# Performance work log

Measured on AMD Instinct MI355X. Metric: run time of the kernel, lower is better.

## Reference

```python
import jax, jax.numpy as jnp
import numpy as np


def _causal_conv(x, w, b, dilation):
    # x: (B, Cin, N), w: (Cout, Cin, K) -> causal: left-pad (K-1)*dilation
    pad = (w.shape[-1] - 1) * dilation
    y = jax.lax.conv_general_dilated(
        x, w, window_strides=(1,), padding=[(pad, 0)],
        rhs_dilation=(dilation,), dimension_numbers=('NCH', 'OIH', 'NCH'))
    return y + b[None, :, None]


def setup_inputs() -> dict:
    key = jax.random.key(0)
    ks = jax.random.split(key, 8)
    B, N, C, L = 8, 32768, 16, 30
    s = 0.1  # weight scale to avoid gate saturation
    return {
        'x': jax.random.normal(ks[0], (B, N), dtype=jnp.float32) * 1000.0,  # int16-like samples
        'lengths': jax.random.randint(ks[1], (B,), N // 2, N),
        'w0': jax.random.normal(ks[2], (C, 1, 2), dtype=jnp.float32) * s,
        'b0': jnp.zeros((C,), jnp.float32),
        'wf': jax.random.normal(ks[3], (L - 1, C, C, 2), dtype=jnp.float32) * s,
        'bf': jnp.zeros((L - 1, C), jnp.float32),
        'wg': jax.random.normal(ks[4], (L - 1, C, C, 2), dtype=jnp.float32) * s,
        'bg': jnp.zeros((L - 1, C), jnp.float32),
        'wa': jax.random.normal(ks[5], (64, C), dtype=jnp.float32) * s,
        'ba': jnp.zeros((64,), jnp.float32),
        'wo': jax.random.normal(ks[6], (256, 64), dtype=jnp.float32) * s,
        'bo': jnp.zeros((256,), jnp.float32),
    }


def reference(x, lengths, w0, b0, wf, bf, wg, bg, wa, ba, wo, bo):
    L = wf.shape[0] + 1  # total layers (layer 0 is plain causal conv)
    xin = (x / 32768.0)[:, None, :]            # (B,1,N), int16 normalization 65536/2
    out0 = _causal_conv(xin, w0, b0, 1)        # (B,C,N)
    agg = out0                                 # skip aggregate
    h = xin + out0                             # residual input (broadcast 1->C channels)
    for i in range(1, L):                      # fixed small layer count
        d = 2 ** (i % 10)
        f = _causal_conv(h, wf[i - 1], bf[i - 1], d)
        g = _causal_conv(h, wg[i - 1], bg[i - 1], d)
        out = jnp.tanh(f) * jax.nn.sigmoid(g)  # gated activation unit
        agg = agg + out
        h = h + out
    a = jnp.einsum('oc,bcn->bon', wa, jax.nn.relu(agg)) + ba[None, :, None]  # agregate1x1
    o = jnp.einsum('oc,bcn->bon', wo, jax.nn.relu(a)) + bo[None, :, None]    # output1x1
    o = jax.nn.log_softmax(o, axis=1)
    mask = (jnp.arange(o.shape[-1]) < lengths[:, None]).astype(o.dtype)      # (B,N)
    return o * mask[:, None, :]
```

## Files before the change

kernel.cpp:

```cpp
#include <hip/hip_runtime.h>

#define NSEQ 32768
#define NB 8
#define NC 16
#define LBLK 1024
#define LPX (LBLK / 8)
#define QGRD 4096
#define QPX (QGRD / 8)

__device__ __forceinline__ float sigm_f(float x) {
    return __fdividef(1.f, 1.f + __expf(-x));
}
__device__ __forceinline__ float tanh_f(float x) {
    return __fdividef(2.f, 1.f + __expf(-2.f * x)) - 1.f;
}

__global__ __launch_bounds__(256) void k_layer0(
    const float* __restrict__ x, const float* __restrict__ w0,
    const float* __restrict__ b0, float* __restrict__ h)
{
    int bid = blockIdx.x;
    int tid = ((bid & 7) * LPX + (bid >> 3)) * 256 + threadIdx.x;
    int n = tid & (NSEQ - 1);
    const float inv = 1.f / 32768.f;
    float xc = x[tid] * inv;
    float xp = (n >= 1) ? x[tid - 1] * inv : 0.f;
    float v[NC];
#pragma unroll
    for (int c = 0; c < NC; c++) {
        float o = w0[c * 2] * xp + w0[c * 2 + 1] * xc + b0[c];
        v[c] = xc + o;
    }
    float4* ph = (float4*)(h + (size_t)tid * NC);
#pragma unroll
    for (int i = 0; i < 4; i++)
        ph[i] = make_float4(v[i * 4], v[i * 4 + 1], v[i * 4 + 2], v[i * 4 + 3]);
}

__global__ __launch_bounds__(256) void k_layer(
    const float* __restrict__ hin, float* __restrict__ hout,
    const float* __restrict__ wf, const float* __restrict__ bf,
    const float* __restrict__ wg, const float* __restrict__ bg, int d)
{
    int bid = blockIdx.x;
    int lbid = (bid & 7) * QPX + (bid >> 3);
    int t = threadIdx.x;
    int pos = lbid * 64 + (t & 63);
    int q = __builtin_amdgcn_readfirstlane(t >> 6);
    int n = pos & (NSEQ - 1);

    float hc[NC], hp[NC];
    {
        const float4* pc = (const float4*)(hin + (size_t)pos * NC);
#pragma unroll
        for (int i = 0; i < 4; i++) {
            float4 tv = pc[i];
            hc[i * 4] = tv.x; hc[i * 4 + 1] = tv.y; hc[i * 4 + 2] = tv.z; hc[i * 4 + 3] = tv.w;
        }
    }
    if (n >= d) {
        const float4* pp = (const float4*)(hin + (size_t)(pos - d) * NC);
#pragma unroll
        for (int i = 0; i < 4; i++) {
            float4 tv = pp[i];
            hp[i * 4] = tv.x; hp[i * 4 + 1] = tv.y; hp[i * 4 + 2] = tv.z; hp[i * 4 + 3] = tv.w;
        }
    } else {
#pragma unroll
        for (int i = 0; i < NC; i++) hp[i] = 0.f;
    }

    const int c0 = q * 4;
    float f[4], g[4];
#pragma unroll
    for (int j = 0; j < 4; j++) { f[j] = bf[c0 + j]; g[j] = bg[c0 + j]; }

#pragma unroll
    for (int ci = 0; ci < NC; ci++) {
        float xp = hp[ci], xc = hc[ci];
#pragma unroll
        for (int j = 0; j < 4; j++) {
            int co = c0 + j;
            f[j] = fmaf(wf[(co * NC + ci) * 2 + 0], xp, f[j]);
            f[j] = fmaf(wf[(co * NC + ci) * 2 + 1], xc, f[j]);
            g[j] = fmaf(wg[(co * NC + ci) * 2 + 0], xp, g[j]);
            g[j] = fmaf(wg[(co * NC + ci) * 2 + 1], xc, g[j]);
        }
    }

    float v[4];
#pragma unroll
    for (int j = 0; j < 4; j++) {
        float outv = tanh_f(f[j]) * sigm_f(g[j]);
        v[j] = hc[c0 + j] + outv;
    }
    float4* po = (float4*)(hout + (size_t)pos * NC + c0);
    po[0] = make_float4(v[0], v[1], v[2], v[3]);
}

__global__ __launch_bounds__(512, 2) void k_final(
    const float* __restrict__ hfin, const float* __restrict__ x,
    const int* __restrict__ lengths,
    const float* __restrict__ wa, const float* __restrict__ ba,
    const float* __restrict__ wo, const float* __restrict__ bo,
    float* __restrict__ out)
{
    __shared__ float s_r[64][17];
    __shared__ float s_ra[64][65];
    __shared__ float s_red[2][8][64];

    int t = threadIdx.x;
    int p = t & 63;
    int q = __builtin_amdgcn_readfirstlane(t >> 6);
    int blk = blockIdx.x;
    int b = blk >> 9;
    int n0 = (blk & 511) << 6;
    int n = n0 + p;
    size_t pos = (size_t)b * NSEQ + n;
    float xin = x[pos] * (1.f / 32768.f);

    if (q < 4) {
        const float4* ph = (const float4*)(hfin + pos * NC);
        float4 v = ph[q];
        s_r[p][q * 4 + 0] = fmaxf(v.x - xin, 0.f);
        s_r[p][q * 4 + 1] = fmaxf(v.y - xin, 0.f);
        s_r[p][q * 4 + 2] = fmaxf(v.z - xin, 0.f);
        s_r[p][q * 4 + 3] = fmaxf(v.w - xin, 0.f);
    }
    __syncthreads();

    {
        float r[NC];
#pragma unroll
        for (int c = 0; c < NC; c++) r[c] = s_r[p][c];
#pragma unroll
        for (int jj = 0; jj < 8; jj++) {
            int j = q * 8 + jj;
            float acc = ba[j];
#pragma unroll
            for (int c = 0; c < NC; c++) acc = fmaf(wa[j * NC + c], r[c], acc);
            s_ra[p][j] = fmaxf(acc, 0.f);
        }
    }
    __syncthreads();

    float ra[64];
#pragma unroll
    for (int j = 0; j < 64; j++) ra[j] = s_ra[p][j];

    float o[32];
    float m = -1e30f;
#pragma unroll 4
    for (int kk = 0; kk < 32; kk++) {
        int k = q * 32 + kk;
        float acc = bo[k];
#pragma unroll
        for (int j = 0; j < 64; j++) acc = fmaf(wo[k * 64 + j], ra[j], acc);
        o[kk] = acc;
        m = fmaxf(m, acc);
    }
    s_red[0][q][p] = m;
    __syncthreads();
    m = fmaxf(fmaxf(fmaxf(s_red[0][0][p], s_red[0][1][p]),
                    fmaxf(s_red[0][2][p], s_red[0][3][p])),
              fmaxf(fmaxf(s_red[0][4][p], s_red[0][5][p]),
                    fmaxf(s_red[0][6][p], s_red[0][7][p])));
    float s = 0.f;
#pragma unroll
    for (int kk = 0; kk < 32; kk++) s += __expf(o[kk] - m);
    s_red[1][q][p] = s;
    __syncthreads();
    s = ((s_red[1][0][p] + s_red[1][1][p]) + (s_red[1][2][p] + s_red[1][3][p]))
      + ((s_red[1][4][p] + s_red[1][5][p]) + (s_red[1][6][p] + s_red[1][7][p]));
    float lse = m + __logf(s);

    bool valid = n < lengths[b];
    float* po = out + ((size_t)b * 256 + q * 32) * NSEQ + n;
#pragma unroll
    for (int kk = 0; kk < 32; kk++) {
        float v = valid ? (o[kk] - lse) : 0.f;
        __builtin_nontemporal_store(v, &po[(size_t)kk * NSEQ]);
    }
}

extern "C" void kernel_launch(void* const* d_in, const int* in_sizes, int n_in,
                              void* d_out, int out_size, void* d_ws, size_t ws_size,
                              hipStream_t stream) {
    const float* x   = (const float*)d_in[0];
    const int* lens  = (const int*)d_in[1];
    const float* w0  = (const float*)d_in[2];
    const float* b0  = (const float*)d_in[3];
    const float* wf  = (const float*)d_in[4];
    const float* bf  = (const float*)d_in[5];
    const float* wg  = (const float*)d_in[6];
    const float* bg  = (const float*)d_in[7];
    const float* wa  = (const float*)d_in[8];
    const float* ba  = (const float*)d_in[9];
    const float* wo  = (const float*)d_in[10];
    const float* bo  = (const float*)d_in[11];
    float* out = (float*)d_out;

    float* hA = (float*)d_ws;
    float* hB = hA + (size_t)NB * NSEQ * NC;

    k_layer0<<<dim3(LBLK), dim3(256), 0, stream>>>(x, w0, b0, hA);

    float* cur = hA;
    float* nxt = hB;
    for (int i = 1; i <= 29; i++) {
        int d = 1 << (i % 10);
        k_layer<<<dim3(QGRD), dim3(256), 0, stream>>>(cur, nxt,
                                         wf + (size_t)(i - 1) * NC * NC * 2,
                                         bf + (size_t)(i - 1) * NC,
                                         wg + (size_t)(i - 1) * NC * NC * 2,
                                         bg + (size_t)(i - 1) * NC, d);
        float* tmp = cur; cur = nxt; nxt = tmp;
    }

    dim3 fgrd(NB * (NSEQ / 64));
    k_final<<<fgrd, dim3(512), 0, stream>>>(cur, x, lens, wa, ba, wo, bo, out);
}
```

Before: 638.5 us.

## Fuse runs of small-dilation layers into one LDS-resident kernel with halo

Adds a k_group kernel that loads a 512-position tile plus a 256-position causal halo into shared memory. It then runs up to eight gated layers in place, with block-wide syncs between layers, before writing the tile back. Three groups cover the layers whose cumulative dilation fits in the halo, and the 256- and 512-dilation layers stay on the original per-layer kernel. This is meant to cut the global read/write round-trips and kernel launches per layer, at the cost of recomputing the halo, lower occupancy from 48KB of LDS and large register arrays, and only 512 blocks per group launch.

```diff
diff --git a/kernel.cpp b/kernel.cpp
--- a/kernel.cpp
+++ b/kernel.cpp
@@ -7,6 +7,9 @@
 #define LPX (LBLK / 8)
 #define QGRD 4096
 #define QPX (QGRD / 8)
+#define GGRD 512
+#define GPX (GGRD / 8)
+#define GBUF 768
 
 __device__ __forceinline__ float sigm_f(float x) {
     return __fdividef(1.f, 1.f + __expf(-x));
@@ -96,6 +99,105 @@
     }
     float4* po = (float4*)(hout + (size_t)pos * NC + c0);
     po[0] = make_float4(v[0], v[1], v[2], v[3]);
+}
+
+__global__ __launch_bounds__(256, 2) void k_group(
+    const float* __restrict__ hin, float* __restrict__ hout,
+    const float* __restrict__ wf, const float* __restrict__ bf,
+    const float* __restrict__ wg, const float* __restrict__ bg,
+    int i0, int nl)
+{
+    __shared__ float hs[NC][GBUF];
+    int bid = blockIdx.x;
+    int blk = (bid & 7) * GPX + (bid >> 3);
+    int t = threadIdx.x;
+    int wb = blk & 63;
+
+#pragma unroll
+    for (int k = 0; k < 3; k++) {
+        int idx = t + k * 256;
+        if (wb > 0 || idx >= 256) {
+            const float4* ph = (const float4*)(hin + ((size_t)blk * 512 + idx - 256) * NC);
+#pragma unroll
+            for (int i4 = 0; i4 < 4; i4++) {
+                float4 tv = ph[i4];
+                hs[i4 * 4 + 0][idx] = tv.x; hs[i4 * 4 + 1][idx] = tv.y;
+                hs[i4 * 4 + 2][idx] = tv.z; hs[i4 * 4 + 3][idx] = tv.w;
+            }
+        } else {
+#pragma unroll
+            for (int c = 0; c < NC; c++) hs[c][idx] = 0.f;
+        }
+    }
+    __syncthreads();
+
+#pragma unroll 1
+    for (int j = 0; j < nl; j++) {
+        const int i = i0 + j;
+        const int d = 1 << (i % 10);
+        const float* wfl = wf + (size_t)(i - 1) * NC * NC * 2;
+        const float* bfl = bf + (size_t)(i - 1) * NC;
+        const float* wgl = wg + (size_t)(i - 1) * NC * NC * 2;
+        const float* bgl = bg + (size_t)(i - 1) * NC;
+
+        float v[3][NC];
+#pragma unroll
+        for (int k = 0; k < 3; k++) {
+            const int idx = t + k * 256;
+            float hc[NC], hp[NC];
+#pragma unroll
+            for (int c = 0; c < NC; c++) hc[c] = hs[c][idx];
+            if (idx >= d) {
+#pragma unroll
+                for (int c = 0; c < NC; c++) hp[c] = hs[c][idx - d];
+            } else {
+#pragma unroll
+                for (int c = 0; c < NC; c++) hp[c] = 0.f;
+            }
+
+            float f[NC], g[NC];
+#pragma unroll
+            for (int co = 0; co < NC; co++) { f[co] = bfl[co]; g[co] = bgl[co]; }
+
+#pragma unroll
+            for (int ci = 0; ci < NC; ci++) {
+                float xp = hp[ci], xc = hc[ci];
+#pragma unroll
+                for (int co = 0; co < NC; co++) {
+                    f[co] = fmaf(wfl[(co * NC + ci) * 2 + 0], xp, f[co]);
+                    f[co] = fmaf(wfl[(co * NC + ci) * 2 + 1], xc, f[co]);
+                    g[co] = fmaf(wgl[(co * NC + ci) * 2 + 0], xp, g[co]);
+                    g[co] = fmaf(wgl[(co * NC + ci) * 2 + 1], xc, g[co]);
+                }
+            }
+
+#pragma unroll
+            for (int co = 0; co < NC; co++) {
+                float outv = tanh_f(f[co]) * sigm_f(g[co]);
+                v[k][co] = hc[co] + outv;
+            }
+        }
+        __syncthreads();
+#pragma unroll
+        for (int k = 0; k < 3; k++) {
+            const int idx = t + k * 256;
+            if (wb > 0 || idx >= 256) {
+#pragma unroll
+                for (int c = 0; c < NC; c++) hs[c][idx] = v[k][c];
+            }
+        }
+        __syncthreads();
+    }
+
+#pragma unroll
+    for (int k = 0; k < 2; k++) {
+        int idx = 256 + t + k * 256;
+        float4* po = (float4*)(hout + ((size_t)blk * 512 + idx - 256) * NC);
+#pragma unroll
+        for (int i4 = 0; i4 < 4; i4++)
+            po[i4] = make_float4(hs[i4 * 4 + 0][idx], hs[i4 * 4 + 1][idx],
+                                 hs[i4 * 4 + 2][idx], hs[i4 * 4 + 3][idx]);
+    }
 }
 
 __global__ __launch_bounds__(512, 2) void k_final(
@@ -203,20 +305,23 @@
     float* hA = (float*)d_ws;
     float* hB = hA + (size_t)NB * NSEQ * NC;
 
+    auto WF = [&](int i) { return wf + (size_t)(i - 1) * NC * NC * 2; };
+    auto BF = [&](int i) { return bf + (size_t)(i - 1) * NC; };
+    auto WG = [&](int i) { return wg + (size_t)(i - 1) * NC * NC * 2; };
+    auto BG = [&](int i) { return bg + (size_t)(i - 1) * NC; };
+
     k_layer0<<<dim3(LBLK), dim3(256), 0, stream>>>(x, w0, b0, hA);
 
-    float* cur = hA;
-    float* nxt = hB;
-    for (int i = 1; i <= 29; i++) {
-        int d = 1 << (i % 10);
-        k_layer<<<dim3(QGRD), dim3(256), 0, stream>>>(cur, nxt,
-                                         wf + (size_t)(i - 1) * NC * NC * 2,
-                                         bf + (size_t)(i - 1) * NC,
-                                         wg + (size_t)(i - 1) * NC * NC * 2,
-                                         bg + (size_t)(i - 1) * NC, d);
-        float* tmp = cur; cur = nxt; nxt = tmp;
-    }
+    k_group<<<dim3(GGRD), dim3(256), 0, stream>>>(hA, hB, wf, bf, wg, bg, 1, 7);
+    k_layer<<<dim3(QGRD), dim3(256), 0, stream>>>(hB, hA, WF(8), BF(8), WG(8), BG(8), 256);
+    k_layer<<<dim3(QGRD), dim3(256), 0, stream>>>(hA, hB, WF(9), BF(9), WG(9), BG(9), 512);
+    k_group<<<dim3(GGRD), dim3(256), 0, stream>>>(hB, hA, wf, bf, wg, bg, 10, 8);
+    k_layer<<<dim3(QGRD), dim3(256), 0, stream>>>(hA, hB, WF(18), BF(18), WG(18), BG(18), 256);
+    k_layer<<<dim3(QGRD), dim3(256), 0, stream>>>(hB, hA, WF(19), BF(19), WG(19), BG(19), 512);
+    k_group<<<dim3(GGRD), dim3(256), 0, stream>>>(hA, hB, wf, bf, wg, bg, 20, 8);
+    k_layer<<<dim3(QGRD), dim3(256), 0, stream>>>(hB, hA, WF(28), BF(28), WG(28), BG(28), 256);
+    k_layer<<<dim3(QGRD), dim3(256), 0, stream>>>(hA, hB, WF(29), BF(29), WG(29), BG(29), 512);
 
     dim3 fgrd(NB * (NSEQ / 64));
-    k_final<<<fgrd, dim3(512), 0, stream>>>(cur, x, lens, wa, ba, wo, bo, out);
-}
+    k_final<<<fgrd, dim3(512), 0, stream>>>(hB, x, lens, wa, ba, wo, bo, out);
+}
```

Result: slower. 1.202 ms (+88.2%).
